# Performance work log

Measured on AMD Instinct MI355X. Metric: run time of the kernel, lower is better.

## Reference

```python
import jax, jax.numpy as jnp
import numpy as np

ALPHA = 0.8      # synaptic current decay
BETA = 0.9       # membrane decay
THR = 1.0        # snntorch default threshold
SURR_ALPHA = 2.0 # snntorch ATan surrogate default

@jax.custom_vjp
def spike_fn(u):
    # heaviside forward, ATan surrogate backward (snntorch default)
    return (u > 0).astype(u.dtype)

def _spike_fwd(u):
    return spike_fn(u), u

def _spike_bwd(u, g):
    return (g * (SURR_ALPHA / 2) / (1 + (jnp.pi / 2 * SURR_ALPHA * u) ** 2),)

spike_fn.defvjp(_spike_fwd, _spike_bwd)

def setup_inputs() -> dict:
    key = jax.random.key(0)
    kx, kw, kb = jax.random.split(key, 3)
    B, T, F = 64, 256, 1024
    x = jax.random.normal(kx, (B, T, F), dtype=jnp.float32)
    W = jax.random.normal(kw, (F, F), dtype=jnp.float32) / np.sqrt(F)  # recurrent Linear weight
    b = jax.random.normal(kb, (F,), dtype=jnp.float32) * 0.01          # recurrent Linear bias
    return {"x": x, "W": W, "b": b}

def reference(x, W, b):
    B, T, F = x.shape

    def step(carry, xt):
        spk, syn, mem = carry
        # reset based on incoming (previous-step) membrane, detached (snntorch)
        reset = jax.lax.stop_gradient((mem > THR).astype(x.dtype))
        syn = ALPHA * syn + xt + spk @ W.T + b          # synaptic current + recurrent drive
        mem = BETA * mem + syn - reset * THR            # subtract reset mechanism
        spk = spike_fn(mem - THR)
        return (spk, syn, mem), (spk, mem)

    z = jnp.zeros((B, F), dtype=x.dtype)
    _, (spk_rec, mem_rec) = jax.lax.scan(step, (z, z, z), jnp.swapaxes(x, 0, 1))
    # [T,B,F] -> [B,T,F]
    return jnp.swapaxes(spk_rec, 0, 1), jnp.swapaxes(mem_rec, 0, 1)
```

## Files before the change

### kernel.cpp

```cpp
#include <hip/hip_runtime.h>


#define NT 512

typedef __bf16 bf16x8 __attribute__((ext_vector_type(8)));
typedef float f32x4 __attribute__((ext_vector_type(4)));
typedef int i32x4 __attribute__((ext_vector_type(4)));

static __device__ __forceinline__ unsigned short f2bf(float v) {
    union { float f; unsigned int u; } a; a.f = v;
    unsigned int u = a.u;
    u += 0x7fffu + ((u >> 16) & 1u);
    return (unsigned short)(u >> 16);
}

static __device__ __forceinline__ void decomp512(float w, int* d) {
    long long v = llround((double)w * 68719476736.0);
    #pragma unroll
    for (int i = 0; i < 4; ++i) {
        int r = (int)(v & 511);
        if (r >= 256) r -= 512;
        d[i] = r;
        v = (v - (long long)r) >> 9;
    }
}

__launch_bounds__(NT, 1)
__global__ void snn_persist_kernel(const float* __restrict__ x,
                                   const float* __restrict__ W,
                                   const float* __restrict__ bias,
                                   float* __restrict__ out,
                                   unsigned int* __restrict__ gbm)
{
    constexpr int T = 256, F = 1024;
    const int bid = blockIdx.x;
    const int js  = bid & 63;
    const int bg  = bid >> 6;
    const int tid = threadIdx.x;
    const int lane = tid & 63;
    const int wv   = tid >> 6;

    __shared__ __align__(16) unsigned int wd0[32*64*4];
    __shared__ __align__(16) unsigned int wd1[32*64*4];
    __shared__ __align__(16) unsigned int wd2[32*64*4];
    __shared__ __align__(16) unsigned int wd3[32*64*4];
    __shared__ unsigned short wbm[8][128];
    __shared__ double partD[8*256];

    for (int it = 0; it < 4; ++it) {
        int s = tid + NT*it;
        int kc = s >> 6, l = s & 63;
        int n = l & 15, q = l >> 4;
        int f0 = kc*32 + q*8;
        const float* wr = W + (size_t)(js*16 + n)*F + f0;
        float e[8];
        *(float4*)&e[0] = *(const float4*)(wr);
        *(float4*)&e[4] = *(const float4*)(wr + 4);
        unsigned int pk0[4], pk1[4], pk2[4], pk3[4];
        #pragma unroll
        for (int i = 0; i < 4; ++i) {
            int da[4], db[4];
            decomp512(e[2*i],   da);
            decomp512(e[2*i+1], db);
            pk0[i] = (unsigned int)f2bf((float)da[0]) | ((unsigned int)f2bf((float)db[0]) << 16);
            pk1[i] = (unsigned int)f2bf((float)da[1]) | ((unsigned int)f2bf((float)db[1]) << 16);
            pk2[i] = (unsigned int)f2bf((float)da[2]) | ((unsigned int)f2bf((float)db[2]) << 16);
            pk3[i] = (unsigned int)f2bf((float)da[3]) | ((unsigned int)f2bf((float)db[3]) << 16);
        }
        #pragma unroll
        for (int i = 0; i < 4; ++i) {
            wd0[s*4+i] = pk0[i]; wd1[s*4+i] = pk1[i];
            wd2[s*4+i] = pk2[i]; wd3[s*4+i] = pk3[i];
        }
    }

    const int brow = ((tid >> 4) & 3)*4 + (tid >> 6);
    const int jcol = tid & 15;
    const int bglob = bg*16 + brow;
    const double bj = (double)bias[js*16 + jcol];
    const size_t obase = (size_t)bglob*T*F + js*16 + jcol;
    float* outspk = out;
    float* outmem = out + (size_t)64*T*F;

    double syn = 0.0, mem = 0.0, rst = 0.0;

    __syncthreads();

    const int q = lane >> 4, r15 = lane & 15;

    for (int t = 0; t < T; ++t) {
        float xv = 0.f;
        if (tid < 256) xv = x[obase + (size_t)t*F];

        double h = 0.0;
        if (t > 0) {
            const unsigned int tg = (unsigned int)t;
            const unsigned int* slot = gbm + (size_t)(((t-1) & 3)*4 + bg)*1024;
            const unsigned int* p0 = slot + wv*128 + lane;
            const unsigned int* p1 = p0 + 64;
            unsigned int v0, v1;
            do {
                v0 = __hip_atomic_load(p0, __ATOMIC_RELAXED, __HIP_MEMORY_SCOPE_AGENT);
                v1 = __hip_atomic_load(p1, __ATOMIC_RELAXED, __HIP_MEMORY_SCOPE_AGENT);
            } while (__any(((v0 >> 16) != tg) | ((v1 >> 16) != tg)));
            wbm[wv][lane]      = (unsigned short)v0;
            wbm[wv][64 + lane] = (unsigned short)v1;

            f32x4 ac0 = {0.f,0.f,0.f,0.f}, ac1 = ac0, ac2 = ac0, ac3 = ac0;
            #pragma unroll
            for (int c4 = 0; c4 < 4; ++c4) {
                int kc = wv*4 + c4;
                unsigned int us = wbm[wv][(2*c4 + (q >> 1))*16 + r15];
                unsigned int byt = (us >> ((q & 1)*8)) & 0xFFu;
                unsigned int d0 = ((byt&1u)  ?0x3F80u:0u) | ((byt&2u)  ?0x3F800000u:0u);
                unsigned int d1 = ((byt&4u)  ?0x3F80u:0u) | ((byt&8u)  ?0x3F800000u:0u);
                unsigned int d2 = ((byt&16u) ?0x3F80u:0u) | ((byt&32u) ?0x3F800000u:0u);
                unsigned int d3 = ((byt&64u) ?0x3F80u:0u) | ((byt&128u)?0x3F800000u:0u);
                i32x4 ai = {(int)d0, (int)d1, (int)d2, (int)d3};
                bf16x8 a = __builtin_bit_cast(bf16x8, ai);
                size_t fo = (size_t)(kc*64 + lane)*4;
                bf16x8 b0 = *(const bf16x8*)(wd0 + fo);
                bf16x8 b1 = *(const bf16x8*)(wd1 + fo);
                bf16x8 b2 = *(const bf16x8*)(wd2 + fo);
                bf16x8 b3 = *(const bf16x8*)(wd3 + fo);
                ac0 = __builtin_amdgcn_mfma_f32_16x16x32_bf16(a, b0, ac0, 0, 0, 0);
                ac1 = __builtin_amdgcn_mfma_f32_16x16x32_bf16(a, b1, ac1, 0, 0, 0);
                ac2 = __builtin_amdgcn_mfma_f32_16x16x32_bf16(a, b2, ac2, 0, 0, 0);
                ac3 = __builtin_amdgcn_mfma_f32_16x16x32_bf16(a, b3, ac3, 0, 0, 0);
            }
            const double c0 = 1.0/68719476736.0;
            const double c1 = 1.0/134217728.0;
            const double c2 = 1.0/262144.0;
            const double c3 = 1.0/512.0;
            #pragma unroll
            for (int r = 0; r < 4; ++r)
                partD[wv*256 + r*64 + lane] =
                    (double)ac0[r]*c0 + (double)ac1[r]*c1 +
                    (double)ac2[r]*c2 + (double)ac3[r]*c3;
            __syncthreads();
            if (tid < 256) {
                #pragma unroll
                for (int w = 0; w < 8; ++w) h += partD[w*256 + tid];
            }
        }
        if (tid < 256) {
            syn = 0.8*syn + (double)xv + h + bj;
            mem = 0.9*mem + syn - rst;
            bool sp = (mem > 1.0);
            unsigned long long m = __ballot(sp);
            if ((lane & 15) == 0) {
                int g = lane >> 4;
                unsigned int word = (unsigned int)((m >> (16*g)) & 0xFFFFull);
                unsigned int val = (((unsigned int)(t + 1)) << 16) | word;
                unsigned int* dst = gbm + (size_t)((t & 3)*4 + bg)*1024 + js*16 + (4*g + wv);
                __hip_atomic_store(dst, val, __ATOMIC_RELAXED, __HIP_MEMORY_SCOPE_AGENT);
            }
            rst = sp ? 1.0 : 0.0;
            outspk[obase + (size_t)t*F] = sp ? 1.0f : 0.0f;
            outmem[obase + (size_t)t*F] = (float)mem;
        }
        __syncthreads();
    }
}

extern "C" void kernel_launch(void* const* d_in, const int* in_sizes, int n_in,
                              void* d_out, int out_size, void* d_ws, size_t ws_size,
                              hipStream_t stream) {
    const float* x    = (const float*)d_in[0];
    const float* W    = (const float*)d_in[1];
    const float* bias = (const float*)d_in[2];
    float* out = (float*)d_out;

    unsigned int* gbm = (unsigned int*)d_ws;

    hipMemsetAsync(d_ws, 0, 65536, stream);
    hipLaunchKernelGGL(snn_persist_kernel, dim3(256), dim3(512), 0, stream,
                       x, W, bias, out, gbm);
}
```

Baseline: 564.3 us.

## Hold decomposed weights in registers, relayout spike bitmap, prefetch x

Keeps the four bf16 digit planes of each block's weight slice in VGPRs instead of LDS, which removes per-step LDS weight loads. The global spike-bitmap layout is permuted so each lane polls the words it needs directly, dropping the LDS staging buffer and an extra sync. The next x value is prefetched during the current step, and the block-index mapping is swapped to bg-minor. A dummy LDS pad, written only under a bias condition, keeps one block per CU, and removing the trailing __syncthreads relies on the remaining barrier to protect partD reuse.

New measurement: 1.705 ms. +202.2%, slower.

```diff
diff --git a/kernel.cpp b/kernel.cpp
--- a/kernel.cpp
+++ b/kernel.cpp
@@ -34,43 +34,42 @@
 {
     constexpr int T = 256, F = 1024;
     const int bid = blockIdx.x;
-    const int js  = bid & 63;
-    const int bg  = bid >> 6;
+    const int bg  = bid & 3;
+    const int js  = bid >> 2;
     const int tid = threadIdx.x;
     const int lane = tid & 63;
     const int wv   = tid >> 6;
+    const int q = lane >> 4, r15 = lane & 15;
+    const int qh = q >> 1, ql = q & 1;
 
-    __shared__ __align__(16) unsigned int wd0[32*64*4];
-    __shared__ __align__(16) unsigned int wd1[32*64*4];
-    __shared__ __align__(16) unsigned int wd2[32*64*4];
-    __shared__ __align__(16) unsigned int wd3[32*64*4];
-    __shared__ unsigned short wbm[8][128];
     __shared__ double partD[8*256];
+    __shared__ double lds_pad[9216];
 
-    for (int it = 0; it < 4; ++it) {
-        int s = tid + NT*it;
-        int kc = s >> 6, l = s & 63;
-        int n = l & 15, q = l >> 4;
-        int f0 = kc*32 + q*8;
-        const float* wr = W + (size_t)(js*16 + n)*F + f0;
+    if (bias[0] > 1.0e30f) lds_pad[tid] = 1.0;
+
+    bf16x8 wreg[4][4];
+    #pragma unroll
+    for (int c4 = 0; c4 < 4; ++c4) {
+        const int kc = wv*4 + c4;
+        const float* wr = W + (size_t)(js*16 + r15)*F + kc*32 + q*8;
         float e[8];
-        *(float4*)&e[0] = *(const float4*)(wr);
+        *(float4*)&e[0] = *(const float4*)wr;
         *(float4*)&e[4] = *(const float4*)(wr + 4);
-        unsigned int pk0[4], pk1[4], pk2[4], pk3[4];
+        unsigned int pk[4][4];
         #pragma unroll
         for (int i = 0; i < 4; ++i) {
             int da[4], db[4];
             decomp512(e[2*i],   da);
             decomp512(e[2*i+1], db);
-            pk0[i] = (unsigned int)f2bf((float)da[0]) | ((unsigned int)f2bf((float)db[0]) << 16);
-            pk1[i] = (unsigned int)f2bf((float)da[1]) | ((unsigned int)f2bf((float)db[1]) << 16);
-            pk2[i] = (unsigned int)f2bf((float)da[2]) | ((unsigned int)f2bf((float)db[2]) << 16);
-            pk3[i] = (unsigned int)f2bf((float)da[3]) | ((unsigned int)f2bf((float)db[3]) << 16);
+            #pragma unroll
+            for (int l = 0; l < 4; ++l)
+                pk[l][i] = (unsigned int)f2bf((float)da[l])
+                         | ((unsigned int)f2bf((float)db[l]) << 16);
         }
         #pragma unroll
-        for (int i = 0; i < 4; ++i) {
-            wd0[s*4+i] = pk0[i]; wd1[s*4+i] = pk1[i];
-            wd2[s*4+i] = pk2[i]; wd3[s*4+i] = pk3[i];
+        for (int l = 0; l < 4; ++l) {
+            i32x4 t4 = {(int)pk[l][0], (int)pk[l][1], (int)pk[l][2], (int)pk[l][3]};
+            wreg[c4][l] = __builtin_bit_cast(bf16x8, t4);
         }
     }
 
@@ -83,55 +82,45 @@
     float* outmem = out + (size_t)64*T*F;
 
     double syn = 0.0, mem = 0.0, rst = 0.0;
+    float xv = (tid < 256) ? x[obase] : 0.f;
 
-    __syncthreads();
-
-    const int q = lane >> 4, r15 = lane & 15;
+    const int gown = (js>>3)*128 + (js&1)*64 + (lane&3)*4 + ((js>>1)&3);
 
     for (int t = 0; t < T; ++t) {
-        float xv = 0.f;
-        if (tid < 256) xv = x[obase + (size_t)t*F];
-
         double h = 0.0;
         if (t > 0) {
             const unsigned int tg = (unsigned int)t;
-            const unsigned int* slot = gbm + (size_t)(((t-1) & 3)*4 + bg)*1024;
-            const unsigned int* p0 = slot + wv*128 + lane;
-            const unsigned int* p1 = p0 + 64;
-            unsigned int v0, v1;
+            const unsigned int* slot = gbm + (size_t)(((t-1)&3)*4 + bg)*1024;
+            const unsigned int* pd = slot + wv*128 + qh*64 + r15*4;
+            const unsigned int* pg = slot + gown;
+            unsigned int w0, w1, w2, w3, g0;
             do {
-                v0 = __hip_atomic_load(p0, __ATOMIC_RELAXED, __HIP_MEMORY_SCOPE_AGENT);
-                v1 = __hip_atomic_load(p1, __ATOMIC_RELAXED, __HIP_MEMORY_SCOPE_AGENT);
-            } while (__any(((v0 >> 16) != tg) | ((v1 >> 16) != tg)));
-            wbm[wv][lane]      = (unsigned short)v0;
-            wbm[wv][64 + lane] = (unsigned short)v1;
+                w0 = __hip_atomic_load(pd+0, __ATOMIC_RELAXED, __HIP_MEMORY_SCOPE_AGENT);
+                w1 = __hip_atomic_load(pd+1, __ATOMIC_RELAXED, __HIP_MEMORY_SCOPE_AGENT);
+                w2 = __hip_atomic_load(pd+2, __ATOMIC_RELAXED, __HIP_MEMORY_SCOPE_AGENT);
+                w3 = __hip_atomic_load(pd+3, __ATOMIC_RELAXED, __HIP_MEMORY_SCOPE_AGENT);
+                g0 = __hip_atomic_load(pg,   __ATOMIC_RELAXED, __HIP_MEMORY_SCOPE_AGENT);
+            } while (__any(((w0>>16)!=tg) | ((w1>>16)!=tg) | ((w2>>16)!=tg) |
+                           ((w3>>16)!=tg) | ((g0>>16)!=tg)));
 
             f32x4 ac0 = {0.f,0.f,0.f,0.f}, ac1 = ac0, ac2 = ac0, ac3 = ac0;
+            unsigned int ww[4] = {w0, w1, w2, w3};
             #pragma unroll
             for (int c4 = 0; c4 < 4; ++c4) {
-                int kc = wv*4 + c4;
-                unsigned int us = wbm[wv][(2*c4 + (q >> 1))*16 + r15];
-                unsigned int byt = (us >> ((q & 1)*8)) & 0xFFu;
+                unsigned int byt = (ww[c4] >> (ql*8)) & 0xFFu;
                 unsigned int d0 = ((byt&1u)  ?0x3F80u:0u) | ((byt&2u)  ?0x3F800000u:0u);
                 unsigned int d1 = ((byt&4u)  ?0x3F80u:0u) | ((byt&8u)  ?0x3F800000u:0u);
                 unsigned int d2 = ((byt&16u) ?0x3F80u:0u) | ((byt&32u) ?0x3F800000u:0u);
                 unsigned int d3 = ((byt&64u) ?0x3F80u:0u) | ((byt&128u)?0x3F800000u:0u);
                 i32x4 ai = {(int)d0, (int)d1, (int)d2, (int)d3};
                 bf16x8 a = __builtin_bit_cast(bf16x8, ai);
-                size_t fo = (size_t)(kc*64 + lane)*4;
-                bf16x8 b0 = *(const bf16x8*)(wd0 + fo);
-                bf16x8 b1 = *(const bf16x8*)(wd1 + fo);
-                bf16x8 b2 = *(const bf16x8*)(wd2 + fo);
-                bf16x8 b3 = *(const bf16x8*)(wd3 + fo);
-                ac0 = __builtin_amdgcn_mfma_f32_16x16x32_bf16(a, b0, ac0, 0, 0, 0);
-                ac1 = __builtin_amdgcn_mfma_f32_16x16x32_bf16(a, b1, ac1, 0, 0, 0);
-                ac2 = __builtin_amdgcn_mfma_f32_16x16x32_bf16(a, b2, ac2, 0, 0, 0);
-                ac3 = __builtin_amdgcn_mfma_f32_16x16x32_bf16(a, b3, ac3, 0, 0, 0);
+                ac0 = __builtin_amdgcn_mfma_f32_16x16x32_bf16(a, wreg[c4][0], ac0, 0,0,0);
+                ac1 = __builtin_amdgcn_mfma_f32_16x16x32_bf16(a, wreg[c4][1], ac1, 0,0,0);
+                ac2 = __builtin_amdgcn_mfma_f32_16x16x32_bf16(a, wreg[c4][2], ac2, 0,0,0);
+                ac3 = __builtin_amdgcn_mfma_f32_16x16x32_bf16(a, wreg[c4][3], ac3, 0,0,0);
             }
-            const double c0 = 1.0/68719476736.0;
-            const double c1 = 1.0/134217728.0;
-            const double c2 = 1.0/262144.0;
-            const double c3 = 1.0/512.0;
+            const double c0 = 1.0/68719476736.0, c1 = 1.0/134217728.0;
+            const double c2 = 1.0/262144.0,      c3 = 1.0/512.0;
             #pragma unroll
             for (int r = 0; r < 4; ++r)
                 partD[wv*256 + r*64 + lane] =
@@ -143,6 +132,10 @@
                 for (int w = 0; w < 8; ++w) h += partD[w*256 + tid];
             }
         }
+
+        float xn = 0.f;
+        if (tid < 256 && t + 1 < T) xn = x[obase + (size_t)(t+1)*F];
+
         if (tid < 256) {
             syn = 0.8*syn + (double)xv + h + bj;
             mem = 0.9*mem + syn - rst;
@@ -150,16 +143,18 @@
             unsigned long long m = __ballot(sp);
             if ((lane & 15) == 0) {
                 int g = lane >> 4;
+                int row = 4*g + wv;
                 unsigned int word = (unsigned int)((m >> (16*g)) & 0xFFFFull);
                 unsigned int val = (((unsigned int)(t + 1)) << 16) | word;
-                unsigned int* dst = gbm + (size_t)((t & 3)*4 + bg)*1024 + js*16 + (4*g + wv);
+                unsigned int* dst = gbm + (size_t)((t&3)*4 + bg)*1024
+                                  + (js>>3)*128 + (js&1)*64 + row*4 + ((js>>1)&3);
                 __hip_atomic_store(dst, val, __ATOMIC_RELAXED, __HIP_MEMORY_SCOPE_AGENT);
             }
             rst = sp ? 1.0 : 0.0;
             outspk[obase + (size_t)t*F] = sp ? 1.0f : 0.0f;
             outmem[obase + (size_t)t*F] = (float)mem;
         }
-        __syncthreads();
+        xv = xn;
     }
 }
 
```
